# Optimization experiments

Hardware: AMD Instinct MI355X
Metric: run time of the kernel (lower is better)

## Reference

```python
import jax, jax.numpy as jnp
import numpy as np

AUDIO_DIM, TEXT_DIM, HIDDEN_DIM = 512, 768, 512
B, AUDIO_LEN, TEXT_LEN = 8, 2048, 512


def setup_inputs() -> dict:
    key = jax.random.key(0)
    ks = jax.random.split(key, 9)
    audio_features = jax.random.normal(ks[0], (B, AUDIO_LEN, AUDIO_DIM), dtype=jnp.float32)
    text_features = jax.random.normal(ks[1], (B, TEXT_LEN, TEXT_DIM), dtype=jnp.float32)
    text_mask = jax.random.randint(ks[2], (B, TEXT_LEN), 0, 2).astype(jnp.int32)
    # Linear params (PyTorch default init scale ~ U(-1/sqrt(fan_in), 1/sqrt(fan_in)))
    def lin(kw, kb, fan_in, fan_out):
        bound = 1.0 / np.sqrt(fan_in)
        W = jax.random.uniform(kw, (fan_in, fan_out), minval=-bound, maxval=bound, dtype=jnp.float32)
        b = jax.random.uniform(kb, (fan_out,), minval=-bound, maxval=bound, dtype=jnp.float32)
        return W, b
    Wq, bq = lin(ks[3], ks[4], AUDIO_DIM, HIDDEN_DIM)
    Wk, bk = lin(ks[5], ks[6], TEXT_DIM, HIDDEN_DIM)
    Wv, bv = lin(ks[7], ks[8], TEXT_DIM, HIDDEN_DIM)
    return {
        "audio_features": audio_features,
        "text_features": text_features,
        "Wq": Wq, "bq": bq, "Wk": Wk, "bk": bk, "Wv": Wv, "bv": bv,
        "text_mask": text_mask,
    }


def reference(audio_features, text_features, Wq, bq, Wk, bk, Wv, bv, text_mask):
    scale = HIDDEN_DIM ** -0.5
    q = jnp.einsum("bad,dh->bah", audio_features, Wq) + bq  # (B, A, H)
    k = jnp.einsum("btd,dh->bth", text_features, Wk) + bk   # (B, T, H)
    v = jnp.einsum("btd,dh->bth", text_features, Wv) + bv   # (B, T, H)
    scores = jnp.einsum("bah,bth->bat", q, k) * scale        # (B, A, T)
    mask = text_mask[:, None, :]  # (B, 1, T)
    scores = jnp.where(mask == 0, -jnp.inf, scores)
    attn = jax.nn.softmax(scores, axis=-1)
    # dropout is identity in eval mode
    enhanced_audio = jnp.einsum("bat,bth->bah", attn, v)     # (B, A, H)
    return enhanced_audio
```

## Files before the change

kernel.cpp:

```cpp
#include <hip/hip_runtime.h>
#include <cstdint>
#include <cstddef>

#define AUDIO_DIM 512
#define TEXT_DIM  768
#define HIDDEN    512
#define BATCH     8
#define ALEN      2048
#define TLEN      512

typedef _Float16 half8 __attribute__((ext_vector_type(8)));
typedef _Float16 half4_t __attribute__((ext_vector_type(4)));
typedef float floatx4 __attribute__((ext_vector_type(4)));

#define AS1 __attribute__((address_space(1)))
#define AS3 __attribute__((address_space(3)))

__device__ __forceinline__ void gload_lds16(const void* g, void* l) {
    __builtin_amdgcn_global_load_lds((const AS1 void*)g, (AS3 void*)l, 16, 0, 0);
}

__device__ __forceinline__ int swz(int r) { return (r >> 1) & 3; }

__global__ __launch_bounds__(256) void prep(
    const float* __restrict__ audio, const float* __restrict__ text,
    const float* __restrict__ Wq, const float* __restrict__ Wk,
    const float* __restrict__ Wv,
    _Float16* __restrict__ audio_h, _Float16* __restrict__ text_h,
    _Float16* __restrict__ Wq_t, _Float16* __restrict__ Wk_t,
    _Float16* __restrict__ Wv_t)
{
    __shared__ _Float16 tt[32 * 33];
    const int bid = blockIdx.x, tid = threadIdx.x;
    if (bid < 11264) {
        const float* src; _Float16* dst; int i;
        if (bid < 8192) { src = audio; dst = audio_h; i = bid * 256 + tid; }
        else            { src = text;  dst = text_h;  i = (bid - 8192) * 256 + tid; }
        float4 v = ((const float4*)src)[i];
        half4_t h;
        h.x = (_Float16)v.x; h.y = (_Float16)v.y; h.z = (_Float16)v.z; h.w = (_Float16)v.w;
        ((half4_t*)dst)[i] = h;
    } else {
        const float* src; _Float16* dst; int R, lb;
        if (bid < 11520)      { lb = bid - 11264; src = Wq; dst = Wq_t; R = 512; }
        else if (bid < 11904) { lb = bid - 11520; src = Wk; dst = Wk_t; R = 768; }
        else                  { lb = bid - 11904; src = Wv; dst = Wv_t; R = 768; }
        const int C = 512;
        const int c0 = (lb & 15) * 32, r0 = (lb >> 4) * 32;
        const int tx = tid & 31, ty = tid >> 5;
#pragma unroll
        for (int i = 0; i < 4; i++) {
            int r = ty + i * 8;
            tt[r * 33 + tx] = (_Float16)src[(size_t)(r0 + r) * C + c0 + tx];
        }
        __syncthreads();
#pragma unroll
        for (int i = 0; i < 4; i++) {
            int r = ty + i * 8;
            dst[(size_t)(c0 + r) * R + r0 + tx] = tt[tx * 33 + r];
        }
    }
}

template <bool OUT16, bool ROWBIAS>
__device__ __forceinline__ void gemm_body(
    const _Float16* __restrict__ A, const _Float16* __restrict__ Bt,
    const float* __restrict__ bias, void* __restrict__ Cp,
    int N, int K, int m0, int n0, _Float16* Asm, _Float16* Bsm)
{
    const int tid = threadIdx.x;
    const int l = tid & 63, w = tid >> 6;
    const int wm = w >> 1, wn = w & 1;
    const int srow = l >> 2, sj = l & 3;
    const int q = l >> 4, c16 = l & 15;

    floatx4 acc[4][4] = {};

    for (int k0 = 0; k0 < K; k0 += 32) {
        if (k0) __syncthreads();
#pragma unroll
        for (int i = 0; i < 2; i++) {
            int rb = (w * 2 + i) * 16;
            int r = rb + srow;
            int cc = sj ^ swz(r);
            gload_lds16(A + (size_t)(m0 + r) * K + k0 + cc * 8, Asm + rb * 32);
            gload_lds16(Bt + (size_t)(n0 + r) * K + k0 + cc * 8, Bsm + rb * 32);
        }
        __syncthreads();

        half8 af[4], bf[4];
#pragma unroll
        for (int t = 0; t < 4; t++) {
            int rA = wm * 64 + t * 16 + c16;
            af[t] = *(const half8*)&Asm[rA * 32 + ((q ^ swz(rA)) << 3)];
            int rB = wn * 64 + t * 16 + c16;
            bf[t] = *(const half8*)&Bsm[rB * 32 + ((q ^ swz(rB)) << 3)];
        }
#pragma unroll
        for (int mi = 0; mi < 4; mi++)
#pragma unroll
            for (int ni = 0; ni < 4; ni++)
                acc[mi][ni] = __builtin_amdgcn_mfma_f32_16x16x32_f16(
                    af[mi], bf[ni], acc[mi][ni], 0, 0, 0);
    }

    if (OUT16) {
        float bcol[4];
        float brow[4][4];
        if (!ROWBIAS) {
#pragma unroll
            for (int ni = 0; ni < 4; ni++)
                bcol[ni] = bias[n0 + wn * 64 + ni * 16 + c16];
        } else {
#pragma unroll
            for (int mi = 0; mi < 4; mi++) {
                float4 b4 = *(const float4*)&bias[m0 + wm * 64 + mi * 16 + q * 4];
                brow[mi][0] = b4.x; brow[mi][1] = b4.y;
                brow[mi][2] = b4.z; brow[mi][3] = b4.w;
            }
        }
        _Float16* C = (_Float16*)Cp;
#pragma unroll
        for (int ni = 0; ni < 4; ni++) {
            int col = n0 + wn * 64 + ni * 16 + c16;
#pragma unroll
            for (int mi = 0; mi < 4; mi++) {
                int row = m0 + wm * 64 + mi * 16 + q * 4;
#pragma unroll
                for (int r = 0; r < 4; r++) {
                    float b = ROWBIAS ? brow[mi][r] : bcol[ni];
                    C[(size_t)(row + r) * N + col] = (_Float16)(acc[mi][ni][r] + b);
                }
            }
        }
    } else {
        float* C = (float*)Cp;
#pragma unroll
        for (int ni = 0; ni < 4; ni++) {
            int col = n0 + wn * 64 + ni * 16 + c16;
#pragma unroll
            for (int mi = 0; mi < 4; mi++) {
                int row = m0 + wm * 64 + mi * 16 + q * 4;
#pragma unroll
                for (int r = 0; r < 4; r++)
                    C[(size_t)(row + r) * N + col] = acc[mi][ni][r];
            }
        }
    }
}

__global__ __launch_bounds__(256, 3) void qkv_gemm(
    const _Float16* __restrict__ audio_h, const _Float16* __restrict__ text_h,
    const _Float16* __restrict__ Wq_t, const _Float16* __restrict__ Wk_t,
    const _Float16* __restrict__ Wv_t,
    const float* __restrict__ bq, const float* __restrict__ bk,
    const float* __restrict__ bv,
    _Float16* __restrict__ Qh, _Float16* __restrict__ Kh,
    _Float16* __restrict__ Vt)
{
    __shared__ __align__(16) _Float16 Asm[128 * 32];
    __shared__ __align__(16) _Float16 Bsm[128 * 32];
    const int bid = blockIdx.x;
    if (bid < 512) {
        int t = (bid & 7) * 64 + (bid >> 3);
        gemm_body<true, false>(audio_h, Wq_t, bq, Qh, 512, 512,
                               (t >> 2) * 128, (t & 3) * 128, Asm, Bsm);
    } else if (bid < 640) {
        int s = bid - 512;
        int t = (s & 7) * 16 + (s >> 3);
        gemm_body<true, false>(text_h, Wk_t, bk, Kh, 512, 768,
                               (t >> 2) * 128, (t & 3) * 128, Asm, Bsm);
    } else {
        int s = bid - 640;
        int t = (s & 7) * 16 + (s >> 3);
        int z = t >> 4, by = (t >> 2) & 3, bx = t & 3;
        gemm_body<true, true>(Wv_t, text_h + (size_t)z * 393216, bv,
                              Vt + (size_t)z * 262144, 512, 768,
                              by * 128, bx * 128, Asm, Bsm);
    }
}

__global__ __launch_bounds__(256, 2) void pv_gemm(
    const _Float16* __restrict__ P, const _Float16* __restrict__ Vt,
    float* __restrict__ out)
{
    __shared__ __align__(16) _Float16 Asm[128 * 32];
    __shared__ __align__(16) _Float16 Bsm[128 * 32];
    const int lin = blockIdx.x;
    const int t = (lin & 7) * 64 + (lin >> 3);
    const int z = t >> 6, by = (t >> 2) & 15, bx = t & 3;
    gemm_body<false, false>(P + (size_t)z * 1048576, Vt + (size_t)z * 262144,
                            nullptr, out + (size_t)z * 1048576, 512, 512,
                            by * 128, bx * 128, Asm, Bsm);
}

__global__ __launch_bounds__(256, 2) void scores_softmax(
    const _Float16* __restrict__ Qh, const _Float16* __restrict__ Kh,
    const int* __restrict__ mask, _Float16* __restrict__ P) {
    __shared__ __align__(16) _Float16 Qs[32 * 32];
    __shared__ __align__(16) _Float16 Ks[512 * 32];
    __shared__ float red[4][32];
    __shared__ float red2[4][32];
    const int tid = threadIdx.x, l = tid & 63, w = tid >> 6;
    const int lin = blockIdx.x;
    const int tb = (lin & 7) * 64 + (lin >> 3);
    const int b = tb >> 6, a0 = (tb & 63) * 32;
    const _Float16* Qb = Qh + (size_t)(b * ALEN + a0) * HIDDEN;
    const _Float16* Kb = Kh + (size_t)b * TLEN * HIDDEN;
    const int srow = l >> 2, sj = l & 3;
    const int q = l >> 4, c16 = l & 15;

    floatx4 acc[2][8] = {};

    for (int k0 = 0; k0 < HIDDEN; k0 += 32) {
        if (k0) __syncthreads();
        if (w < 2) {
            int rb = w * 16;
            int r = rb + srow;
            int cc = sj ^ swz(r);
            gload_lds16(Qb + (size_t)r * HIDDEN + k0 + cc * 8, &Qs[rb * 32]);
        }
#pragma unroll
        for (int i = 0; i < 8; i++) {
            int rb = (w * 8 + i) * 16;
            int r = rb + srow;
            int cc = sj ^ swz(r);
            gload_lds16(Kb + (size_t)r * HIDDEN + k0 + cc * 8, &Ks[rb * 32]);
        }
        __syncthreads();

        half8 af[2], bf[8];
#pragma unroll
        for (int t = 0; t < 2; t++) {
            int rA = t * 16 + c16;
            af[t] = *(const half8*)&Qs[rA * 32 + ((q ^ swz(rA)) << 3)];
        }
#pragma unroll
        for (int t = 0; t < 8; t++) {
            int rB = w * 128 + t * 16 + c16;
            bf[t] = *(const half8*)&Ks[rB * 32 + ((q ^ swz(rB)) << 3)];
        }
#pragma unroll
        for (int mi = 0; mi < 2; mi++)
#pragma unroll
            for (int ni = 0; ni < 8; ni++)
                acc[mi][ni] = __builtin_amdgcn_mfma_f32_16x16x32_f16(
                    af[mi], bf[ni], acc[mi][ni], 0, 0, 0);
    }

    const float scale = 0.044194173824159216f;
    int mv[8];
#pragma unroll
    for (int ni = 0; ni < 8; ni++)
        mv[ni] = mask[b * TLEN + w * 128 + ni * 16 + c16];
#pragma unroll
    for (int mi = 0; mi < 2; mi++)
#pragma unroll
        for (int ni = 0; ni < 8; ni++)
#pragma unroll
            for (int r = 0; r < 4; r++)
                acc[mi][ni][r] = mv[ni] ? acc[mi][ni][r] * scale : -1e30f;

    float mx[2][4];
#pragma unroll
    for (int mi = 0; mi < 2; mi++)
#pragma unroll
        for (int r = 0; r < 4; r++) {
            float m = -1e30f;
#pragma unroll
            for (int ni = 0; ni < 8; ni++) m = fmaxf(m, acc[mi][ni][r]);
#pragma unroll
            for (int off = 1; off <= 8; off <<= 1) m = fmaxf(m, __shfl_xor(m, off));
            mx[mi][r] = m;
        }
    if (c16 == 0)
#pragma unroll
        for (int mi = 0; mi < 2; mi++)
#pragma unroll
            for (int r = 0; r < 4; r++) red[w][mi * 16 + q * 4 + r] = mx[mi][r];
    __syncthreads();
#pragma unroll
    for (int mi = 0; mi < 2; mi++)
#pragma unroll
        for (int r = 0; r < 4; r++) {
            int row = mi * 16 + q * 4 + r;
            mx[mi][r] = fmaxf(fmaxf(red[0][row], red[1][row]),
                              fmaxf(red[2][row], red[3][row]));
        }

    float sm[2][4];
#pragma unroll
    for (int mi = 0; mi < 2; mi++)
#pragma unroll
        for (int r = 0; r < 4; r++) {
            float s = 0.f;
#pragma unroll
            for (int ni = 0; ni < 8; ni++) {
                float e = __expf(acc[mi][ni][r] - mx[mi][r]);
                acc[mi][ni][r] = e;
                s += e;
            }
#pragma unroll
            for (int off = 1; off <= 8; off <<= 1) s += __shfl_xor(s, off);
            sm[mi][r] = s;
        }
    if (c16 == 0)
#pragma unroll
        for (int mi = 0; mi < 2; mi++)
#pragma unroll
            for (int r = 0; r < 4; r++) red2[w][mi * 16 + q * 4 + r] = sm[mi][r];
    __syncthreads();

    _Float16* Pb = P + (size_t)(b * ALEN + a0) * TLEN;
#pragma unroll
    for (int mi = 0; mi < 2; mi++)
#pragma unroll
        for (int r = 0; r < 4; r++) {
            int row = mi * 16 + q * 4 + r;
            float inv = 1.f / (red2[0][row] + red2[1][row] + red2[2][row] + red2[3][row]);
#pragma unroll
            for (int ni = 0; ni < 8; ni++)
                Pb[(size_t)row * TLEN + w * 128 + ni * 16 + c16] =
                    (_Float16)(acc[mi][ni][r] * inv);
        }
}

extern "C" void kernel_launch(void* const* d_in, const int* in_sizes, int n_in,
                              void* d_out, int out_size, void* d_ws, size_t ws_size,
                              hipStream_t stream)
{
    const float* audio = (const float*)d_in[0];
    const float* text  = (const float*)d_in[1];
    const float* Wq    = (const float*)d_in[2];
    const float* bq    = (const float*)d_in[3];
    const float* Wk    = (const float*)d_in[4];
    const float* bk    = (const float*)d_in[5];
    const float* Wv    = (const float*)d_in[6];
    const float* bv    = (const float*)d_in[7];
    const int*   maskp = (const int*)d_in[8];
    float* out = (float*)d_out;

    _Float16* audio_h = (_Float16*)d_out;
    _Float16* Qh      = audio_h + (size_t)8388608;

    _Float16* ws16   = (_Float16*)d_ws;
    _Float16* text_h = ws16;
    _Float16* Wq_t   = text_h + 3145728;
    _Float16* Wk_t   = Wq_t + 262144;
    _Float16* Wv_t   = Wk_t + 393216;
    _Float16* Kh     = Wv_t + 393216;
    _Float16* Vt     = Kh + 2097152;
    _Float16* P      = Vt + 2097152;

    prep<<<12288, 256, 0, stream>>>(audio, text, Wq, Wk, Wv,
                                    audio_h, text_h, Wq_t, Wk_t, Wv_t);
    qkv_gemm<<<768, 256, 0, stream>>>(audio_h, text_h, Wq_t, Wk_t, Wv_t,
                                      bq, bk, bv, Qh, Kh, Vt);
    scores_softmax<<<512, 256, 0, stream>>>(Qh, Kh, maskp, P);
    pv_gemm<<<512, 256, 0, stream>>>(P, Vt, out);
}
```

Measured before the change: 169.5 us.

## Fuse scores-softmax and PV GEMM into one attention kernel keeping P in LDS

Merges the scores/softmax kernel and the P·V GEMM into a single attention kernel. The normalized probabilities stay in shared memory instead of round-tripping through a global fp16 P buffer, and the whole 32x512 Q tile is loaded into LDS once. K and V fragments are now read directly from global memory into registers rather than staged through LDS. This removes one launch and the P write and read, but exposes global-load latency inside the MFMA loops with no explicit prefetch.

```diff
diff --git a/kernel.cpp b/kernel.cpp
--- a/kernel.cpp
+++ b/kernel.cpp
@@ -180,25 +180,12 @@
     }
 }
 
-__global__ __launch_bounds__(256, 2) void pv_gemm(
-    const _Float16* __restrict__ P, const _Float16* __restrict__ Vt,
+__global__ __launch_bounds__(256, 2) void attn(
+    const _Float16* __restrict__ Qh, const _Float16* __restrict__ Kh,
+    const _Float16* __restrict__ Vt, const int* __restrict__ mask,
     float* __restrict__ out)
 {
-    __shared__ __align__(16) _Float16 Asm[128 * 32];
-    __shared__ __align__(16) _Float16 Bsm[128 * 32];
-    const int lin = blockIdx.x;
-    const int t = (lin & 7) * 64 + (lin >> 3);
-    const int z = t >> 6, by = (t >> 2) & 15, bx = t & 3;
-    gemm_body<false, false>(P + (size_t)z * 1048576, Vt + (size_t)z * 262144,
-                            nullptr, out + (size_t)z * 1048576, 512, 512,
-                            by * 128, bx * 128, Asm, Bsm);
-}
-
-__global__ __launch_bounds__(256, 2) void scores_softmax(
-    const _Float16* __restrict__ Qh, const _Float16* __restrict__ Kh,
-    const int* __restrict__ mask, _Float16* __restrict__ P) {
-    __shared__ __align__(16) _Float16 Qs[32 * 32];
-    __shared__ __align__(16) _Float16 Ks[512 * 32];
+    __shared__ __align__(16) _Float16 Qs[32 * 512];
     __shared__ float red[4][32];
     __shared__ float red2[4][32];
     const int tid = threadIdx.x, l = tid & 63, w = tid >> 6;
@@ -207,38 +194,30 @@
     const int b = tb >> 6, a0 = (tb & 63) * 32;
     const _Float16* Qb = Qh + (size_t)(b * ALEN + a0) * HIDDEN;
     const _Float16* Kb = Kh + (size_t)b * TLEN * HIDDEN;
-    const int srow = l >> 2, sj = l & 3;
+    const _Float16* Vb = Vt + (size_t)b * TLEN * HIDDEN;
     const int q = l >> 4, c16 = l & 15;
 
+#pragma unroll
+    for (int i = 0; i < 8; i++) {
+        int r = w * 8 + i;
+        gload_lds16(Qb + (size_t)r * 512 + ((l ^ (r & 7)) << 3), &Qs[r * 512]);
+    }
+    __syncthreads();
+
     floatx4 acc[2][8] = {};
-
-    for (int k0 = 0; k0 < HIDDEN; k0 += 32) {
-        if (k0) __syncthreads();
-        if (w < 2) {
-            int rb = w * 16;
-            int r = rb + srow;
-            int cc = sj ^ swz(r);
-            gload_lds16(Qb + (size_t)r * HIDDEN + k0 + cc * 8, &Qs[rb * 32]);
-        }
-#pragma unroll
-        for (int i = 0; i < 8; i++) {
-            int rb = (w * 8 + i) * 16;
-            int r = rb + srow;
-            int cc = sj ^ swz(r);
-            gload_lds16(Kb + (size_t)r * HIDDEN + k0 + cc * 8, &Ks[rb * 32]);
-        }
-        __syncthreads();
-
+#pragma unroll
+    for (int ks = 0; ks < 16; ks++) {
+        const int k0 = ks * 32;
         half8 af[2], bf[8];
 #pragma unroll
         for (int t = 0; t < 2; t++) {
             int rA = t * 16 + c16;
-            af[t] = *(const half8*)&Qs[rA * 32 + ((q ^ swz(rA)) << 3)];
+            af[t] = *(const half8*)&Qs[rA * 512 + ((((k0 >> 3) + q) ^ (rA & 7)) << 3)];
         }
 #pragma unroll
         for (int t = 0; t < 8; t++) {
             int rB = w * 128 + t * 16 + c16;
-            bf[t] = *(const half8*)&Ks[rB * 32 + ((q ^ swz(rB)) << 3)];
+            bf[t] = *(const half8*)&Kb[(size_t)rB * 512 + k0 + q * 8];
         }
 #pragma unroll
         for (int mi = 0; mi < 2; mi++)
@@ -310,8 +289,7 @@
 #pragma unroll
             for (int r = 0; r < 4; r++) red2[w][mi * 16 + q * 4 + r] = sm[mi][r];
     __syncthreads();
-
-    _Float16* Pb = P + (size_t)(b * ALEN + a0) * TLEN;
+    _Float16* Ps = Qs;
 #pragma unroll
     for (int mi = 0; mi < 2; mi++)
 #pragma unroll
@@ -319,10 +297,49 @@
             int row = mi * 16 + q * 4 + r;
             float inv = 1.f / (red2[0][row] + red2[1][row] + red2[2][row] + red2[3][row]);
 #pragma unroll
+            for (int ni = 0; ni < 8; ni++) {
+                int col = w * 128 + ni * 16 + c16;
+                Ps[row * 512 + ((((col >> 3) ^ (row & 7)) << 3) + (col & 7))] =
+                    (_Float16)(acc[mi][ni][r] * inv);
+            }
+        }
+    __syncthreads();
+
+    floatx4 oacc[2][8] = {};
+#pragma unroll
+    for (int ts = 0; ts < 16; ts++) {
+        const int t0 = ts * 32;
+        half8 af[2], bf[8];
+#pragma unroll
+        for (int t = 0; t < 2; t++) {
+            int rA = t * 16 + c16;
+            af[t] = *(const half8*)&Ps[rA * 512 + ((((t0 >> 3) + q) ^ (rA & 7)) << 3)];
+        }
+#pragma unroll
+        for (int h = 0; h < 8; h++) {
+            int rB = w * 128 + h * 16 + c16;
+            bf[h] = *(const half8*)&Vb[(size_t)rB * 512 + t0 + q * 8];
+        }
+#pragma unroll
+        for (int mi = 0; mi < 2; mi++)
+#pragma unroll
             for (int ni = 0; ni < 8; ni++)
-                Pb[(size_t)row * TLEN + w * 128 + ni * 16 + c16] =
-                    (_Float16)(acc[mi][ni][r] * inv);
-        }
+                oacc[mi][ni] = __builtin_amdgcn_mfma_f32_16x16x32_f16(
+                    af[mi], bf[ni], oacc[mi][ni], 0, 0, 0);
+    }
+
+    float* Ob = out + (size_t)(b * ALEN + a0) * HIDDEN;
+#pragma unroll
+    for (int ni = 0; ni < 8; ni++) {
+        int col = w * 128 + ni * 16 + c16;
+#pragma unroll
+        for (int mi = 0; mi < 2; mi++) {
+            int row = mi * 16 + q * 4;
+#pragma unroll
+            for (int r = 0; r < 4; r++)
+                Ob[(size_t)(row + r) * HIDDEN + col] = oacc[mi][ni][r];
+        }
+    }
 }
 
 extern "C" void kernel_launch(void* const* d_in, const int* in_sizes, int n_in,
@@ -350,12 +367,10 @@
     _Float16* Wv_t   = Wk_t + 393216;
     _Float16* Kh     = Wv_t + 393216;
     _Float16* Vt     = Kh + 2097152;
-    _Float16* P      = Vt + 2097152;
 
     prep<<<12288, 256, 0, stream>>>(audio, text, Wq, Wk, Wv,
                                     audio_h, text_h, Wq_t, Wk_t, Wv_t);
     qkv_gemm<<<768, 256, 0, stream>>>(audio_h, text_h, Wq_t, Wk_t, Wv_t,
                                       bq, bk, bv, Qh, Kh, Vt);
-    scores_softmax<<<512, 256, 0, stream>>>(Qh, Kh, maskp, P);
-    pv_gemm<<<512, 256, 0, stream>>>(P, Vt, out);
-}
+    attn<<<512, 256, 0, stream>>>(Qh, Kh, Vt, maskp, out);
+}
```

Result: slower. 199.5 us (+17.7%).
